# Optimization experiments

Hardware: AMD Instinct MI355X
Metric: run time of the kernel (lower is better)

The kernel has to match this reference:

```python
import jax, jax.numpy as jnp
import numpy as np
from jax import lax

EPS = 1e-10
BN_EPS = 1e-5
T = 0.1
K = 64
B, D, H, Z = 2048, 2048, 512, 500


def _bn(x, g, b):
    # training-mode BatchNorm1d: biased batch stats over axis 0
    mu = x.mean(axis=0)
    var = ((x - mu) ** 2).mean(axis=0)
    return g * (x - mu) / jnp.sqrt(var + BN_EPS) + b


def _leaky(x):
    return jnp.where(x >= 0, x, 0.01 * x)


def setup_inputs() -> dict:
    key = jax.random.key(0)
    ks = jax.random.split(key, 16)
    def lin(k, fan_in, shape):
        return jax.random.normal(k, shape, jnp.float32) / np.sqrt(fan_in)
    return {
        'x': jax.random.uniform(ks[0], (B, D), jnp.float32),
        'u_gumbel': jax.random.uniform(ks[1], (B, D), jnp.float32),
        'eps': jax.random.normal(ks[2], (B, Z), jnp.float32),
        'wc_w1': lin(ks[3], D, (D, H)), 'wc_b1': jnp.zeros((H,)),
        'wc_g': jnp.ones((H,)), 'wc_beta': jnp.zeros((H,)),
        'wc_w2': lin(ks[4], H, (H, D)), 'wc_b2': jnp.zeros((D,)),
        'enc_w1': lin(ks[5], D, (D, 2 * H)), 'enc_b1': jnp.zeros((2 * H,)),
        'enc_g1': jnp.ones((2 * H,)), 'enc_beta1': jnp.zeros((2 * H,)),
        'enc_w2': lin(ks[6], 2 * H, (2 * H, H)), 'enc_b2': jnp.zeros((H,)),
        'enc_g2': jnp.ones((H,)), 'enc_beta2': jnp.zeros((H,)),
        'enc_w3': lin(ks[7], H, (H, H)), 'enc_b3': jnp.zeros((H,)),
        'enc_g3': jnp.ones((H,)), 'enc_beta3': jnp.zeros((H,)),
        'fc21_w': lin(ks[8], H, (H, Z)), 'fc21_b': jnp.zeros((Z,)),
        'fc22_w': lin(ks[9], H, (H, Z)), 'fc22_b': jnp.zeros((Z,)),
        'fc3_w': lin(ks[10], Z, (Z, H)), 'fc3_b': jnp.zeros((H,)),
        'fc3_g': jnp.ones((H,)), 'fc3_beta': jnp.zeros((H,)),
        'fc4_w': lin(ks[11], H, (H, D)), 'fc4_b': jnp.zeros((D,)),
    }


def _sample_subset(w_logits, u):
    # gumbel_keys: w += log(-log(u')) with u' in (EPS, 1)
    u = (1.0 - EPS) * u + EPS
    w = w_logits + jnp.log(-jnp.log(u))

    def step(carry, _):
        w, onehot, acc = carry
        khot_mask = jnp.maximum(1.0 - onehot, EPS)
        w = w + jnp.log(khot_mask)
        onehot = jax.nn.softmax(w / T, axis=-1)
        return (w, onehot, acc + onehot), None

    init = (w, jnp.zeros_like(w), jnp.zeros_like(w))
    (_, _, khot), _ = lax.scan(step, init, None, length=K)
    return khot


def reference(x, u_gumbel, eps,
              wc_w1, wc_b1, wc_g, wc_beta, wc_w2, wc_b2,
              enc_w1, enc_b1, enc_g1, enc_beta1,
              enc_w2, enc_b2, enc_g2, enc_beta2,
              enc_w3, enc_b3, enc_g3, enc_beta3,
              fc21_w, fc21_b, fc22_w, fc22_b,
              fc3_w, fc3_b, fc3_g, fc3_beta, fc4_w, fc4_b):
    # weight_creator: Linear -> BN -> ReLU -> Linear
    h = jax.nn.relu(_bn(x @ wc_w1 + wc_b1, wc_g, wc_beta))
    w_logits = h @ wc_w2 + wc_b2
    khot = _sample_subset(w_logits, u_gumbel)  # [B, D]
    xm = x * khot
    h1 = _leaky(_bn(xm @ enc_w1 + enc_b1, enc_g1, enc_beta1))
    h1 = _leaky(_bn(h1 @ enc_w2 + enc_b2, enc_g2, enc_beta2))
    h1 = _leaky(_bn(h1 @ enc_w3 + enc_b3, enc_g3, enc_beta3))
    mu = h1 @ fc21_w + fc21_b
    logvar = h1 @ fc22_w + fc22_b
    z = mu + eps * jnp.exp(0.5 * logvar)
    hd = _leaky(_bn(z @ fc3_w + fc3_b, fc3_g, fc3_beta))
    mu_x = jax.nn.sigmoid(hd @ fc4_w + fc4_b)
    return (mu_x, mu, logvar)
```

## Files before the change

### kernel.cpp

```cpp
#include <hip/hip_runtime.h>
#include <hip/hip_bf16.h>
#include <math.h>

#define B_DIM 2048
#define D_DIM 2048
#define H_DIM 512
#define Z_DIM 500

#define ACT_NONE 0
#define ACT_RELU 1
#define ACT_SIGMOID 2
#define ACT_LEAKY 3

typedef __attribute__((ext_vector_type(8))) _Float16 f16x8;
typedef __attribute__((ext_vector_type(4))) _Float16 f16x4;
typedef __attribute__((ext_vector_type(4))) float f32x4;
typedef __attribute__((ext_vector_type(2))) float f32x2;

__device__ __forceinline__ float rfl(float x) {
    return __uint_as_float(__builtin_amdgcn_readfirstlane(__float_as_uint(x)));
}

template<int BM, int BN, int TERMS, int BK>
__global__ __launch_bounds__(256, 2) void gemm_f16(
    const _Float16* __restrict__ Ah_, const _Float16* __restrict__ Al_,
    const _Float16* __restrict__ Bh_, const _Float16* __restrict__ Bl_,
    const float* __restrict__ bias, float* __restrict__ C,
    float* __restrict__ part, int M, int N, int K, int act, int Kc)
{
    constexpr int LDK = 40;
    constexpr int NPL = (TERMS == 3) ? 2 : 1;
    constexpr int NCH = BK / 32;
    constexpr int PSA = BM * LDK, PSB = BN * LDK;
    constexpr int CHUNK = NPL * (PSA + PSB);
    constexpr int BUF = NCH * CHUNK;
    constexpr int MT = BM / 32, NT = BN / 32;
    constexpr int CA = BM / 64, CB = BN / 64;
    __shared__ _Float16 smem[2 * BUF];

    const int t = threadIdx.x, lane = t & 63, wv = t >> 6;
    const int wrow = wv >> 1, wcol = wv & 1;
    const int row0 = blockIdx.y * BM, col0 = blockIdx.x * BN;
    const int ks = blockIdx.z * Kc;
    const int nk = Kc / BK;

    f16x8 rA[NCH][CA][NPL], rB[NCH][CB][NPL];

    auto gload = [&](int kt) {
        #pragma unroll
        for (int ch = 0; ch < NCH; ++ch) {
            int kc = kt + ch * 32;
            #pragma unroll
            for (int i = 0; i < CA; ++i) {
                int id = t + i * 256;
                int r = id >> 2, ko = (id & 3) * 8;
                size_t off = (size_t)(row0 + r) * K + kc + ko;
                rA[ch][i][0] = *(const f16x8*)(Ah_ + off);
                if constexpr (TERMS == 3) rA[ch][i][1] = *(const f16x8*)(Al_ + off);
            }
            #pragma unroll
            for (int i = 0; i < CB; ++i) {
                int id = t + i * 256;
                int r = id >> 2, ko = (id & 3) * 8;
                size_t off = (size_t)(col0 + r) * K + kc + ko;
                rB[ch][i][0] = *(const f16x8*)(Bh_ + off);
                if constexpr (TERMS == 3) rB[ch][i][1] = *(const f16x8*)(Bl_ + off);
            }
        }
    };
    auto cstore = [&](int b) {
        #pragma unroll
        for (int ch = 0; ch < NCH; ++ch) {
            _Float16* base = smem + b * BUF + ch * CHUNK;
            #pragma unroll
            for (int i = 0; i < CA; ++i) {
                int id = t + i * 256;
                int r = id >> 2, ko = (id & 3) * 8;
                *(f16x8*)&base[r * LDK + ko] = rA[ch][i][0];
                if constexpr (TERMS == 3) *(f16x8*)&base[PSA + r * LDK + ko] = rA[ch][i][1];
            }
            _Float16* bb = base + NPL * PSA;
            #pragma unroll
            for (int i = 0; i < CB; ++i) {
                int id = t + i * 256;
                int r = id >> 2, ko = (id & 3) * 8;
                *(f16x8*)&bb[r * LDK + ko] = rB[ch][i][0];
                if constexpr (TERMS == 3) *(f16x8*)&bb[PSB + r * LDK + ko] = rB[ch][i][1];
            }
        }
    };

    f32x4 acc[MT][NT];
    #pragma unroll
    for (int i = 0; i < MT; ++i)
        #pragma unroll
        for (int j = 0; j < NT; ++j) {
            f32x4 z = {0.f, 0.f, 0.f, 0.f};
            acc[i][j] = z;
        }

    const int q8 = (lane >> 4) * 8, fr = lane & 15;

    gload(ks);
    cstore(0);
    __syncthreads();

    for (int it = 0; it < nk; ++it) {
        int cur = it & 1;
        if (it + 1 < nk) gload(ks + (it + 1) * BK);

        #pragma unroll
        for (int ch = 0; ch < NCH; ++ch) {
            const _Float16* A0 = smem + cur * BUF + ch * CHUNK;
            const _Float16* A1 = A0 + PSA;
            const _Float16* B0 = A0 + NPL * PSA;
            const _Float16* B1 = B0 + PSB;
            f16x8 ah[MT], al[MT], bh[NT], bl[NT];
            #pragma unroll
            for (int i = 0; i < MT; ++i) {
                int r = wrow * (BM / 2) + i * 16 + fr;
                ah[i] = *(const f16x8*)&A0[r * LDK + q8];
                if constexpr (TERMS == 3) al[i] = *(const f16x8*)&A1[r * LDK + q8];
            }
            #pragma unroll
            for (int j = 0; j < NT; ++j) {
                int n = wcol * (BN / 2) + j * 16 + fr;
                bh[j] = *(const f16x8*)&B0[n * LDK + q8];
                if constexpr (TERMS == 3) bl[j] = *(const f16x8*)&B1[n * LDK + q8];
            }
            #pragma unroll
            for (int i = 0; i < MT; ++i)
                #pragma unroll
                for (int j = 0; j < NT; ++j) {
                    acc[i][j] = __builtin_amdgcn_mfma_f32_16x16x32_f16(ah[i], bh[j], acc[i][j], 0, 0, 0);
                    if constexpr (TERMS == 3) {
                        acc[i][j] = __builtin_amdgcn_mfma_f32_16x16x32_f16(ah[i], bl[j], acc[i][j], 0, 0, 0);
                        acc[i][j] = __builtin_amdgcn_mfma_f32_16x16x32_f16(al[i], bh[j], acc[i][j], 0, 0, 0);
                    }
                }
        }

        if (it + 1 < nk) cstore(cur ^ 1);
        __syncthreads();
    }

    const bool dopart = (gridDim.z > 1);
    float* dst = dopart ? (part + (size_t)blockIdx.z * M * N) : C;
    #pragma unroll
    for (int i = 0; i < MT; ++i) {
        int rbase = row0 + wrow * (BM / 2) + i * 16 + (lane >> 4) * 4;
        #pragma unroll
        for (int j = 0; j < NT; ++j) {
            int c = col0 + wcol * (BN / 2) + j * 16 + (lane & 15);
            if (c < N) {
                float b = dopart ? 0.f : bias[c];
                #pragma unroll
                for (int q = 0; q < 4; ++q) {
                    float v = acc[i][j][q] + b;
                    if (!dopart && act == ACT_SIGMOID)
                        v = 1.f / (1.f + __builtin_amdgcn_exp2f(-v * 1.44269504f));
                    dst[(size_t)(rbase + q) * N + c] = v;
                }
            }
        }
    }
}

__global__ __launch_bounds__(256) void cvt_split_x(
    const float* __restrict__ x, _Float16* __restrict__ xh,
    _Float16* __restrict__ xl, int n4)
{
    int i = blockIdx.x * 256 + threadIdx.x;
    if (i >= n4) return;
    float4 v = ((const float4*)x)[i];
    f16x4 h, l;
    h[0]=(_Float16)v.x; l[0]=(_Float16)(v.x-(float)h[0]);
    h[1]=(_Float16)v.y; l[1]=(_Float16)(v.y-(float)h[1]);
    h[2]=(_Float16)v.z; l[2]=(_Float16)(v.z-(float)h[2]);
    h[3]=(_Float16)v.w; l[3]=(_Float16)(v.w-(float)h[3]);
    ((f16x4*)xh)[i] = h;
    ((f16x4*)xl)[i] = l;
}

__global__ __launch_bounds__(256) void cvt_w_t(
    const float* __restrict__ in, _Float16* __restrict__ outh,
    _Float16* __restrict__ outl, int K, int N, int Kp)
{
    __shared__ float tile[32][33];
    const int t = threadIdx.x;
    const int tk0 = blockIdx.x * 32, tn0 = blockIdx.y * 32;
    const int lx = t & 31, ly = t >> 5;
    #pragma unroll
    for (int r = 0; r < 4; ++r) {
        int k = tk0 + ly + r * 8, n = tn0 + lx;
        tile[ly + r * 8][lx] = (k < K && n < N) ? in[(size_t)k * N + n] : 0.f;
    }
    __syncthreads();
    #pragma unroll
    for (int r = 0; r < 4; ++r) {
        int n = tn0 + ly + r * 8, k = tk0 + lx;
        float v = tile[lx][ly + r * 8];
        _Float16 h = (_Float16)v;
        outh[(size_t)n * Kp + k] = h;
        if (outl) outl[(size_t)n * Kp + k] = (_Float16)(v - (float)h);
    }
}

__global__ __launch_bounds__(256) void reduce_heads(
    const float* __restrict__ part, int S,
    const float* __restrict__ b21, const float* __restrict__ b22,
    float* __restrict__ mu, float* __restrict__ lv)
{
    int i = blockIdx.x * 256 + threadIdx.x;
    const int MN = B_DIM * 1024;
    if (i >= MN) return;
    int row = i >> 10, c = i & 1023;
    float s = 0.f;
    for (int k = 0; k < S; ++k) s += part[(size_t)k * MN + i];
    if (c < Z_DIM) {
        mu[(size_t)row * Z_DIM + c] = s + b21[c];
    } else if (c >= 512 && c < 512 + Z_DIM) {
        lv[(size_t)row * Z_DIM + (c - 512)] = s + b22[c - 512];
    }
}

__global__ __launch_bounds__(256) void reduce_stats(
    const float* __restrict__ part, int S, int Brows, int N, int rowsPerBlock,
    const float* __restrict__ bias, float* __restrict__ Y,
    float* __restrict__ statp)
{
    const int t = threadIdx.x;
    const int col = blockIdx.x * 64 + (t & 63);
    const int g = blockIdx.y;
    const int r0 = g * rowsPerBlock;
    const int r1 = min(r0 + rowsPerBlock, Brows);
    const size_t MN = (size_t)Brows * N;
    const float b = bias[col];
    float s = 0.f, s2 = 0.f;
    for (int r = r0 + (t >> 6); r < r1; r += 4) {
        float v = b;
        for (int k = 0; k < S; ++k) v += part[k * MN + (size_t)r * N + col];
        Y[(size_t)r * N + col] = v;
        s += v;
        s2 += v * v;
    }
    __shared__ float ss[4][64], ss2[4][64];
    ss[t >> 6][t & 63] = s;
    ss2[t >> 6][t & 63] = s2;
    __syncthreads();
    if (t < 64) {
        s  = ss[0][t] + ss[1][t] + ss[2][t] + ss[3][t];
        s2 = ss2[0][t] + ss2[1][t] + ss2[2][t] + ss2[3][t];
        float* p = statp + ((size_t)g * N + col) * 2;
        p[0] = s;
        p[1] = s2;
    }
}

__global__ __launch_bounds__(256) void colstats_final(
    const float* __restrict__ part, int G, int N, int Brows,
    const float* __restrict__ gamma, const float* __restrict__ beta,
    float* __restrict__ scale, float* __restrict__ shift)
{
    int c = blockIdx.x * 256 + threadIdx.x;
    if (c >= N) return;
    float s = 0.f, s2 = 0.f;
    for (int g = 0; g < G; ++g) {
        s  += part[((size_t)g * N + c) * 2];
        s2 += part[((size_t)g * N + c) * 2 + 1];
    }
    float invB = 1.f / (float)Brows;
    float mean = s * invB;
    float var  = s2 * invB - mean * mean;
    float rstd = rsqrtf(var + 1e-5f);
    float sc = gamma[c] * rstd;
    scale[c] = sc;
    shift[c] = beta[c] - mean * sc;
}

__global__ __launch_bounds__(256) void bn_apply_f16(
    const float* __restrict__ Y, const float* __restrict__ scale,
    const float* __restrict__ shift, _Float16* __restrict__ oh,
    _Float16* __restrict__ ol, int total, int N, int act)
{
    int idx = blockIdx.x * 256 + threadIdx.x;
    int i4 = idx * 4;
    if (i4 >= total) return;
    float4 y = *(const float4*)(Y + i4);
    int c = i4 % N;
    float4 sc = *(const float4*)(scale + c);
    float4 sh = *(const float4*)(shift + c);
    float r[4];
    r[0] = y.x * sc.x + sh.x;
    r[1] = y.y * sc.y + sh.y;
    r[2] = y.z * sc.z + sh.z;
    r[3] = y.w * sc.w + sh.w;
    #pragma unroll
    for (int q = 0; q < 4; ++q) {
        if (act == ACT_RELU) r[q] = fmaxf(r[q], 0.f);
        else if (act == ACT_LEAKY) r[q] = (r[q] >= 0.f) ? r[q] : 0.01f * r[q];
    }
    f16x4 h;
    #pragma unroll
    for (int q = 0; q < 4; ++q) h[q] = (_Float16)r[q];
    ((f16x4*)oh)[idx] = h;
    if (ol) {
        f16x4 l;
        #pragma unroll
        for (int q = 0; q < 4; ++q) l[q] = (_Float16)(r[q] - (float)h[q]);
        ((f16x4*)ol)[idx] = l;
    }
}

__global__ __launch_bounds__(256) void gumbel_scan(
    const float* __restrict__ WLg, const float* __restrict__ U,
    const float* __restrict__ X, _Float16* __restrict__ XM)
{
    const int row = blockIdx.x;
    const int t = threadIdx.x, wv = t >> 6, lane = t & 63;
    const float* wrow = WLg + (size_t)row * D_DIM + 8 * t;
    const float* urow = U + (size_t)row * D_DIM + 8 * t;
    const float* xrow = X + (size_t)row * D_DIM + 8 * t;
    _Float16* xmrow = XM + (size_t)row * D_DIM + 8 * t;

    const float L2E = 1.4426950408889634f;
    const float LOG2LN2 = -0.5287663729448977f;

    __shared__ f32x2 sLS[2][4];
    __shared__ float sM0[4];

    f32x2 W2[4], e2[4], acc2[4];

    auto mkW = [&](float wl, float uu) -> float {
        float u = fmaf(uu, 1.0f - 1e-10f, 1e-10f);
        float tl = -__builtin_amdgcn_logf(u);
        return __builtin_amdgcn_exp2f(fmaf(wl, L2E, __builtin_amdgcn_logf(tl) + LOG2LN2));
    };

    {
        float4 ua = *(const float4*)urow, ub = *(const float4*)(urow + 4);
        float4 wa = *(const float4*)wrow, wb = *(const float4*)(wrow + 4);
        W2[0] = f32x2{mkW(wa.x, ua.x), mkW(wa.y, ua.y)};
        W2[1] = f32x2{mkW(wa.z, ua.z), mkW(wa.w, ua.w)};
        W2[2] = f32x2{mkW(wb.x, ub.x), mkW(wb.y, ub.y)};
        W2[3] = f32x2{mkW(wb.z, ub.z), mkW(wb.w, ub.w)};
    }
    #pragma unroll
    for (int j = 0; j < 4; ++j) {
        e2[j] = f32x2{0.f, 0.f};
        acc2[j] = f32x2{0.f, 0.f};
    }

    float rm_s;
    {
        float lm = 0.f;
        #pragma unroll
        for (int j = 0; j < 4; ++j)
            lm = fmaxf(lm, fmaxf(W2[j].x, W2[j].y));
        #pragma unroll
        for (int off = 32; off; off >>= 1)
            lm = fmaxf(lm, __shfl_xor(lm, off));
        if (lane == 0) sM0[wv] = lm;
        __syncthreads();
        float m = fmaxf(fmaxf(sM0[0], sM0[1]), fmaxf(sM0[2], sM0[3]));
        rm_s = rfl(__builtin_amdgcn_rcpf(m));
    }

    float inv_s = 0.f;
    int gi = 0;

    auto iterate = [&](bool refresh) {
        const int p = gi & 1;
        ++gi;
        f32x2 lmv = f32x2{0.f, 0.f}, sv = f32x2{0.f, 0.f};
        #pragma unroll
        for (int j = 0; j < 4; ++j) {
            acc2[j].x = fmaf(e2[j].x, inv_s, acc2[j].x);
            acc2[j].y = fmaf(e2[j].y, inv_s, acc2[j].y);
            f32x2 msk;
            msk.x = fmaxf(fmaf(-e2[j].x, inv_s, 1.0f), 1e-10f);
            msk.y = fmaxf(fmaf(-e2[j].y, inv_s, 1.0f), 1e-10f);
            f32x2 Wn = W2[j] * msk;
            W2[j] = Wn;
            f32x2 r;
            r.x = Wn.x * rm_s;
            r.y = Wn.y * rm_s;
            f32x2 q2 = r * r;
            f32x2 q4 = q2 * q2;
            f32x2 q8 = q4 * q4;
            f32x2 ee = q8 * q2;
            e2[j] = ee;
            sv += ee;
            if (refresh) {
                lmv.x = fmaxf(lmv.x, Wn.x);
                lmv.y = fmaxf(lmv.y, Wn.y);
            }
        }
        float s = sv.x + sv.y;
        if (refresh) {
            float lm = fmaxf(lmv.x, lmv.y);
            #pragma unroll
            for (int off = 32; off; off >>= 1) {
                s += __shfl_xor(s, off);
                lm = fmaxf(lm, __shfl_xor(lm, off));
            }
            if (lane == 0) sLS[p][wv] = f32x2{lm, s};
            __syncthreads();
            f32x2 r0 = sLS[p][0], r1 = sLS[p][1], r2 = sLS[p][2], r3 = sLS[p][3];
            float m = fmaxf(fmaxf(r0.x, r1.x), fmaxf(r2.x, r3.x));
            float st = (r0.y + r1.y) + (r2.y + r3.y);
            rm_s = rfl(__builtin_amdgcn_rcpf(m));
            inv_s = rfl(__builtin_amdgcn_rcpf(st));
        } else {
            #pragma unroll
            for (int off = 32; off; off >>= 1)
                s += __shfl_xor(s, off);
            if (lane == 0) sLS[p][wv].y = s;
            __syncthreads();
            float st = (sLS[p][0].y + sLS[p][1].y) + (sLS[p][2].y + sLS[p][3].y);
            inv_s = rfl(__builtin_amdgcn_rcpf(st));
        }
    };

    for (int ot = 0; ot < 16; ++ot) {
        iterate(false);
        iterate(false);
        iterate(false);
        iterate(true);
    }

    {
        float4 xa = *(const float4*)xrow, xb = *(const float4*)(xrow + 4);
        f32x2 a0, a1, a2, a3;
        a0.x = fmaf(e2[0].x, inv_s, acc2[0].x); a0.y = fmaf(e2[0].y, inv_s, acc2[0].y);
        a1.x = fmaf(e2[1].x, inv_s, acc2[1].x); a1.y = fmaf(e2[1].y, inv_s, acc2[1].y);
        a2.x = fmaf(e2[2].x, inv_s, acc2[2].x); a2.y = fmaf(e2[2].y, inv_s, acc2[2].y);
        a3.x = fmaf(e2[3].x, inv_s, acc2[3].x); a3.y = fmaf(e2[3].y, inv_s, acc2[3].y);
        f16x8 o;
        o[0] = (_Float16)(xa.x * a0.x);
        o[1] = (_Float16)(xa.y * a0.y);
        o[2] = (_Float16)(xa.z * a1.x);
        o[3] = (_Float16)(xa.w * a1.y);
        o[4] = (_Float16)(xb.x * a2.x);
        o[5] = (_Float16)(xb.y * a2.y);
        o[6] = (_Float16)(xb.z * a3.x);
        o[7] = (_Float16)(xb.w * a3.y);
        *(f16x8*)xmrow = o;
    }
}

__global__ __launch_bounds__(256) void z_kernel16(
    const float* __restrict__ mu, const float* __restrict__ lv,
    const float* __restrict__ eps, _Float16* __restrict__ zb, int n4)
{
    int i = blockIdx.x * 256 + threadIdx.x;
    if (i >= n4) return;
    int f = i * 4;
    int row = f / Z_DIM, col = f - row * Z_DIM;
    float4 m = *(const float4*)(mu + f);
    float4 l = *(const float4*)(lv + f);
    float4 e = *(const float4*)(eps + f);
    const float HL2E = 0.7213475204444817f;
    f16x4 r;
    r[0] = (_Float16)(m.x + e.x * __builtin_amdgcn_exp2f(l.x * HL2E));
    r[1] = (_Float16)(m.y + e.y * __builtin_amdgcn_exp2f(l.y * HL2E));
    r[2] = (_Float16)(m.z + e.z * __builtin_amdgcn_exp2f(l.z * HL2E));
    r[3] = (_Float16)(m.w + e.w * __builtin_amdgcn_exp2f(l.w * HL2E));
    *(f16x4*)(zb + (size_t)row * 512 + col) = r;
}

extern "C" void kernel_launch(void* const* d_in, const int* in_sizes, int n_in,
                              void* d_out, int out_size, void* d_ws, size_t ws_size,
                              hipStream_t stream) {
    const float* x        = (const float*)d_in[0];
    const float* u_gumbel = (const float*)d_in[1];
    const float* eps      = (const float*)d_in[2];
    const float* wc_w1    = (const float*)d_in[3];
    const float* wc_b1    = (const float*)d_in[4];
    const float* wc_g     = (const float*)d_in[5];
    const float* wc_beta  = (const float*)d_in[6];
    const float* wc_w2    = (const float*)d_in[7];
    const float* wc_b2    = (const float*)d_in[8];
    const float* enc_w1   = (const float*)d_in[9];
    const float* enc_b1   = (const float*)d_in[10];
    const float* enc_g1   = (const float*)d_in[11];
    const float* enc_beta1= (const float*)d_in[12];
    const float* enc_w2   = (const float*)d_in[13];
    const float* enc_b2   = (const float*)d_in[14];
    const float* enc_g2   = (const float*)d_in[15];
    const float* enc_beta2= (const float*)d_in[16];
    const float* enc_w3   = (const float*)d_in[17];
    const float* enc_b3   = (const float*)d_in[18];
    const float* enc_g3   = (const float*)d_in[19];
    const float* enc_beta3= (const float*)d_in[20];
    const float* fc21_w   = (const float*)d_in[21];
    const float* fc21_b   = (const float*)d_in[22];
    const float* fc22_w   = (const float*)d_in[23];
    const float* fc22_b   = (const float*)d_in[24];
    const float* fc3_w    = (const float*)d_in[25];
    const float* fc3_b    = (const float*)d_in[26];
    const float* fc3_g    = (const float*)d_in[27];
    const float* fc3_beta = (const float*)d_in[28];
    const float* fc4_w    = (const float*)d_in[29];
    const float* fc4_b    = (const float*)d_in[30];

    float* out   = (float*)d_out;
    float* mu_x  = out;
    float* mu    = out + (size_t)B_DIM * D_DIM;
    float* lv    = mu + (size_t)B_DIM * Z_DIM;

    const size_t F1M = 1u << 20;
    float* wsf = (float*)d_ws;
    float*     P_WL  = wsf;
    _Float16*  xh    = (_Float16*)(wsf + 4 * F1M);
    _Float16*  xl    = (_Float16*)(wsf + 6 * F1M);
    _Float16*  xm16  = (_Float16*)(wsf + 4 * F1M);
    float*     Yb    = wsf + 6 * F1M;
    _Float16*  a2    = (_Float16*)(wsf + 8 * F1M);
    _Float16*  a3    = (_Float16*)(wsf + 9 * F1M);
    _Float16*  a4    = (_Float16*)(wsf + 9 * F1M + F1M / 2);
    _Float16*  zb16  = (_Float16*)(wsf + 10 * F1M);
    _Float16*  a5    = (_Float16*)(wsf + 10 * F1M + F1M / 2);
    float*     Hbuf  = wsf + 11 * F1M;
    _Float16*  Hh    = (_Float16*)(wsf + 12 * F1M);
    _Float16*  Hl    = (_Float16*)(wsf + 12 * F1M + F1M / 2);
    _Float16*  w1th  = (_Float16*)(wsf + 13 * F1M);
    _Float16*  w1tl  = (_Float16*)(wsf + 13 * F1M + F1M / 2);
    _Float16*  w2th  = (_Float16*)(wsf + 14 * F1M);
    _Float16*  w2tl  = (_Float16*)(wsf + 14 * F1M + F1M / 2);
    _Float16*  e1t   = (_Float16*)(wsf + 15 * F1M);
    _Float16*  e2t   = (_Float16*)(wsf + 16 * F1M);
    _Float16*  e3t   = (_Float16*)(wsf + 16 * F1M + F1M / 4);
    _Float16*  f21t  = (_Float16*)(wsf + 16 * F1M + 3 * (F1M / 8));
    _Float16*  f22t  = (_Float16*)(wsf + 16 * F1M + 4 * (F1M / 8));
    _Float16*  f3t   = (_Float16*)(wsf + 16 * F1M + 5 * (F1M / 8));
    _Float16*  f4t   = (_Float16*)(wsf + 16 * F1M + 6 * (F1M / 8));
    float*     bnp   = wsf + 17 * F1M + F1M / 4;
    float*     scale = bnp + 131072;
    float*     shift = scale + 2048;

    const int G = 64;

    auto gemm3 = [&](const _Float16* Ah, const _Float16* Al,
                     const _Float16* Bh, const _Float16* Bl,
                     const float* b, float* C, float* part,
                     int N, int K, int SK) {
        dim3 grid((N + 63) / 64, B_DIM / 128, SK);
        gemm_f16<128, 64, 3, 32><<<grid, 256, 0, stream>>>(Ah, Al, Bh, Bl, b, C, part,
                                                           B_DIM, N, K, ACT_NONE, K / SK);
    };
    auto gemm1 = [&](const _Float16* Ah, const _Float16* Bh,
                     const float* b, float* C, float* part,
                     int N, int K, int act, int SK) {
        dim3 grid((N + 63) / 64, B_DIM / 128, SK);
        gemm_f16<128, 64, 1, 64><<<grid, 256, 0, stream>>>(Ah, nullptr, Bh, nullptr, b, C,
                                                           part, B_DIM, N, K, act, K / SK);
    };
    auto bnFromParts = [&](const float* part, int S, const float* b,
                           const float* g_, const float* beta_,
                           float* Y, _Float16* oh, _Float16* ol, int N, int act) {
        dim3 gp(N / 64, G);
        reduce_stats<<<gp, 256, 0, stream>>>(part, S, B_DIM, N, B_DIM / G, b, Y, bnp);
        colstats_final<<<(N + 255) / 256, 256, 0, stream>>>(bnp, G, N, B_DIM, g_, beta_, scale, shift);
        int total = B_DIM * N;
        bn_apply_f16<<<(total / 4 + 255) / 256, 256, 0, stream>>>(Y, scale, shift, oh, ol, total, N, act);
    };
    auto cvtw = [&](const float* in, _Float16* oh, _Float16* ol, int K, int N, int Kp, int Np) {
        dim3 grid(Kp / 32, Np / 32);
        cvt_w_t<<<grid, 256, 0, stream>>>(in, oh, ol, K, N, Kp);
    };

    cvt_split_x<<<4096, 256, 0, stream>>>(x, xh, xl, B_DIM * D_DIM / 4);
    cvtw(wc_w1, w1th, w1tl, 2048, 512, 2048, 512);
    cvtw(wc_w2, w2th, w2tl, 512, 2048, 512, 2048);
    cvtw(enc_w1, e1t, nullptr, 2048, 1024, 2048, 1024);
    cvtw(enc_w2, e2t, nullptr, 1024, 512, 1024, 512);
    cvtw(enc_w3, e3t, nullptr, 512, 512, 512, 512);
    cvtw(fc21_w, f21t, nullptr, 512, 500, 512, 512);
    cvtw(fc22_w, f22t, nullptr, 512, 500, 512, 512);
    cvtw(fc3_w, f3t, nullptr, 500, 512, 512, 512);
    cvtw(fc4_w, f4t, nullptr, 512, 2048, 512, 2048);

    gemm3(xh, xl, w1th, w1tl, nullptr, nullptr, P_WL, 512, 2048, 4);
    bnFromParts(P_WL, 4, wc_b1, wc_g, wc_beta, Hbuf, Hh, Hl, 512, ACT_RELU);
    gemm3(Hh, Hl, w2th, w2tl, wc_b2, P_WL, nullptr, 2048, 512, 1);

    gumbel_scan<<<B_DIM, 256, 0, stream>>>(P_WL, u_gumbel, x, xm16);

    gemm1(xm16, e1t, nullptr, nullptr, P_WL, 1024, 2048, ACT_NONE, 2);
    bnFromParts(P_WL, 2, enc_b1, enc_g1, enc_beta1, Yb, a2, nullptr, 1024, ACT_LEAKY);
    gemm1(a2, e2t, nullptr, nullptr, P_WL, 512, 1024, ACT_NONE, 4);
    bnFromParts(P_WL, 4, enc_b2, enc_g2, enc_beta2, Yb, a3, nullptr, 512, ACT_LEAKY);
    gemm1(a3, e3t, nullptr, nullptr, P_WL, 512, 512, ACT_NONE, 4);
    bnFromParts(P_WL, 4, enc_b3, enc_g3, enc_beta3, Yb, a4, nullptr, 512, ACT_LEAKY);

    gemm1(a4, f21t, nullptr, nullptr, P_WL, 1024, 512, ACT_NONE, 4);
    {
        int MN = B_DIM * 1024;
        reduce_heads<<<(MN + 255) / 256, 256, 0, stream>>>(P_WL, 4, fc21_b, fc22_b, mu, lv);
    }

    hipMemsetAsync(zb16, 0, (size_t)B_DIM * 512 * sizeof(_Float16), stream);
    int n4 = B_DIM * Z_DIM / 4;
    z_kernel16<<<(n4 + 255) / 256, 256, 0, stream>>>(mu, lv, eps, zb16, n4);

    gemm1(zb16, f3t, nullptr, nullptr, P_WL, 512, 512, ACT_NONE, 4);
    bnFromParts(P_WL, 4, fc3_b, fc3_g, fc3_beta, Yb, a5, nullptr, 512, ACT_LEAKY);
    gemm1(a5, f4t, fc4_b, mu_x, nullptr, 2048, 512, ACT_SIGMOID, 1);
}
```

Measured before the change: 422.3 us.

## Process two rows per gumbel-scan block and fuse head reduction with z sampling

```diff
diff --git a/kernel.cpp b/kernel.cpp
--- a/kernel.cpp
+++ b/kernel.cpp
@@ -206,21 +206,31 @@
     }
 }
 
-__global__ __launch_bounds__(256) void reduce_heads(
+__global__ __launch_bounds__(256) void reduce_heads_z(
     const float* __restrict__ part, int S,
     const float* __restrict__ b21, const float* __restrict__ b22,
-    float* __restrict__ mu, float* __restrict__ lv)
+    const float* __restrict__ eps, float* __restrict__ mu,
+    float* __restrict__ lv, _Float16* __restrict__ zb)
 {
     int i = blockIdx.x * 256 + threadIdx.x;
-    const int MN = B_DIM * 1024;
-    if (i >= MN) return;
-    int row = i >> 10, c = i & 1023;
-    float s = 0.f;
-    for (int k = 0; k < S; ++k) s += part[(size_t)k * MN + i];
+    if (i >= B_DIM * 512) return;
+    int row = i >> 9, c = i & 511;
     if (c < Z_DIM) {
-        mu[(size_t)row * Z_DIM + c] = s + b21[c];
-    } else if (c >= 512 && c < 512 + Z_DIM) {
-        lv[(size_t)row * Z_DIM + (c - 512)] = s + b22[c - 512];
+        const size_t MN = (size_t)B_DIM * 1024;
+        size_t ia = (size_t)row * 1024 + c;
+        float sm = b21[c], sl = b22[c];
+        for (int k = 0; k < S; ++k) {
+            sm += part[k * MN + ia];
+            sl += part[k * MN + ia + 512];
+        }
+        size_t o = (size_t)row * Z_DIM + c;
+        mu[o] = sm;
+        lv[o] = sl;
+        const float HL2E = 0.7213475204444817f;
+        zb[(size_t)row * 512 + c] =
+            (_Float16)(sm + eps[o] * __builtin_amdgcn_exp2f(sl * HL2E));
+    } else {
+        zb[(size_t)row * 512 + c] = (_Float16)0.f;
     }
 }
 
@@ -316,20 +326,21 @@
     const float* __restrict__ WLg, const float* __restrict__ U,
     const float* __restrict__ X, _Float16* __restrict__ XM)
 {
-    const int row = blockIdx.x;
     const int t = threadIdx.x, wv = t >> 6, lane = t & 63;
-    const float* wrow = WLg + (size_t)row * D_DIM + 8 * t;
-    const float* urow = U + (size_t)row * D_DIM + 8 * t;
-    const float* xrow = X + (size_t)row * D_DIM + 8 * t;
-    _Float16* xmrow = XM + (size_t)row * D_DIM + 8 * t;
+    const size_t base = (size_t)(blockIdx.x * 2) * D_DIM + 8 * t;
+    const float* wA = WLg + base;  const float* wB = wA + D_DIM;
+    const float* uA = U + base;    const float* uB = uA + D_DIM;
+    const float* xA = X + base;    const float* xB = xA + D_DIM;
+    _Float16* oA = XM + base;      _Float16* oB = oA + D_DIM;
 
     const float L2E = 1.4426950408889634f;
     const float LOG2LN2 = -0.5287663729448977f;
 
-    __shared__ f32x2 sLS[2][4];
-    __shared__ float sM0[4];
-
-    f32x2 W2[4], e2[4], acc2[4];
+    __shared__ f32x4 sLS[2][4];
+    __shared__ f32x2 sM0[4];
+
+    f32x2 WA[4], eA[4], aA[4];
+    f32x2 WB[4], eB[4], aB[4];
 
     auto mkW = [&](float wl, float uu) -> float {
         float u = fmaf(uu, 1.0f - 1e-10f, 1e-10f);
@@ -338,87 +349,110 @@
     };
 
     {
-        float4 ua = *(const float4*)urow, ub = *(const float4*)(urow + 4);
-        float4 wa = *(const float4*)wrow, wb = *(const float4*)(wrow + 4);
-        W2[0] = f32x2{mkW(wa.x, ua.x), mkW(wa.y, ua.y)};
-        W2[1] = f32x2{mkW(wa.z, ua.z), mkW(wa.w, ua.w)};
-        W2[2] = f32x2{mkW(wb.x, ub.x), mkW(wb.y, ub.y)};
-        W2[3] = f32x2{mkW(wb.z, ub.z), mkW(wb.w, ub.w)};
+        float4 u4a = *(const float4*)uA, u4b = *(const float4*)(uA + 4);
+        float4 w4a = *(const float4*)wA, w4b = *(const float4*)(wA + 4);
+        WA[0] = f32x2{mkW(w4a.x, u4a.x), mkW(w4a.y, u4a.y)};
+        WA[1] = f32x2{mkW(w4a.z, u4a.z), mkW(w4a.w, u4a.w)};
+        WA[2] = f32x2{mkW(w4b.x, u4b.x), mkW(w4b.y, u4b.y)};
+        WA[3] = f32x2{mkW(w4b.z, u4b.z), mkW(w4b.w, u4b.w)};
+        u4a = *(const float4*)uB; u4b = *(const float4*)(uB + 4);
+        w4a = *(const float4*)wB; w4b = *(const float4*)(wB + 4);
+        WB[0] = f32x2{mkW(w4a.x, u4a.x), mkW(w4a.y, u4a.y)};
+        WB[1] = f32x2{mkW(w4a.z, u4a.z), mkW(w4a.w, u4a.w)};
+        WB[2] = f32x2{mkW(w4b.x, u4b.x), mkW(w4b.y, u4b.y)};
+        WB[3] = f32x2{mkW(w4b.z, u4b.z), mkW(w4b.w, u4b.w)};
     }
     #pragma unroll
     for (int j = 0; j < 4; ++j) {
-        e2[j] = f32x2{0.f, 0.f};
-        acc2[j] = f32x2{0.f, 0.f};
-    }
-
-    float rm_s;
+        eA[j] = f32x2{0.f, 0.f}; aA[j] = f32x2{0.f, 0.f};
+        eB[j] = f32x2{0.f, 0.f}; aB[j] = f32x2{0.f, 0.f};
+    }
+
+    float rmA, rmB;
     {
-        float lm = 0.f;
-        #pragma unroll
-        for (int j = 0; j < 4; ++j)
-            lm = fmaxf(lm, fmaxf(W2[j].x, W2[j].y));
-        #pragma unroll
-        for (int off = 32; off; off >>= 1)
-            lm = fmaxf(lm, __shfl_xor(lm, off));
-        if (lane == 0) sM0[wv] = lm;
+        float la = 0.f, lb = 0.f;
+        #pragma unroll
+        for (int j = 0; j < 4; ++j) {
+            la = fmaxf(la, fmaxf(WA[j].x, WA[j].y));
+            lb = fmaxf(lb, fmaxf(WB[j].x, WB[j].y));
+        }
+        #pragma unroll
+        for (int off = 32; off; off >>= 1) {
+            la = fmaxf(la, __shfl_xor(la, off));
+            lb = fmaxf(lb, __shfl_xor(lb, off));
+        }
+        if (lane == 0) sM0[wv] = f32x2{la, lb};
         __syncthreads();
-        float m = fmaxf(fmaxf(sM0[0], sM0[1]), fmaxf(sM0[2], sM0[3]));
-        rm_s = rfl(__builtin_amdgcn_rcpf(m));
-    }
-
-    float inv_s = 0.f;
+        f32x2 m0 = sM0[0], m1 = sM0[1], m2 = sM0[2], m3 = sM0[3];
+        rmA = rfl(__builtin_amdgcn_rcpf(fmaxf(fmaxf(m0.x, m1.x), fmaxf(m2.x, m3.x))));
+        rmB = rfl(__builtin_amdgcn_rcpf(fmaxf(fmaxf(m0.y, m1.y), fmaxf(m2.y, m3.y))));
+    }
+
+    float invA = 0.f, invB = 0.f;
     int gi = 0;
 
     auto iterate = [&](bool refresh) {
         const int p = gi & 1;
         ++gi;
-        f32x2 lmv = f32x2{0.f, 0.f}, sv = f32x2{0.f, 0.f};
+        f32x2 lvA = f32x2{0.f, 0.f}, svA = f32x2{0.f, 0.f};
+        f32x2 lvB = f32x2{0.f, 0.f}, svB = f32x2{0.f, 0.f};
         #pragma unroll
         for (int j = 0; j < 4; ++j) {
-            acc2[j].x = fmaf(e2[j].x, inv_s, acc2[j].x);
-            acc2[j].y = fmaf(e2[j].y, inv_s, acc2[j].y);
-            f32x2 msk;
-            msk.x = fmaxf(fmaf(-e2[j].x, inv_s, 1.0f), 1e-10f);
-            msk.y = fmaxf(fmaf(-e2[j].y, inv_s, 1.0f), 1e-10f);
-            f32x2 Wn = W2[j] * msk;
-            W2[j] = Wn;
+            aA[j].x = fmaf(eA[j].x, invA, aA[j].x);
+            aA[j].y = fmaf(eA[j].y, invA, aA[j].y);
+            f32x2 mk;
+            mk.x = fmaxf(fmaf(-eA[j].x, invA, 1.0f), 1e-10f);
+            mk.y = fmaxf(fmaf(-eA[j].y, invA, 1.0f), 1e-10f);
+            f32x2 Wn = WA[j] * mk;
+            WA[j] = Wn;
             f32x2 r;
-            r.x = Wn.x * rm_s;
-            r.y = Wn.y * rm_s;
-            f32x2 q2 = r * r;
-            f32x2 q4 = q2 * q2;
-            f32x2 q8 = q4 * q4;
+            r.x = Wn.x * rmA; r.y = Wn.y * rmA;
+            f32x2 q2 = r * r, q4 = q2 * q2, q8 = q4 * q4;
             f32x2 ee = q8 * q2;
-            e2[j] = ee;
-            sv += ee;
-            if (refresh) {
-                lmv.x = fmaxf(lmv.x, Wn.x);
-                lmv.y = fmaxf(lmv.y, Wn.y);
-            }
-        }
-        float s = sv.x + sv.y;
+            eA[j] = ee;
+            svA += ee;
+            if (refresh) { lvA.x = fmaxf(lvA.x, Wn.x); lvA.y = fmaxf(lvA.y, Wn.y); }
+            aB[j].x = fmaf(eB[j].x, invB, aB[j].x);
+            aB[j].y = fmaf(eB[j].y, invB, aB[j].y);
+            mk.x = fmaxf(fmaf(-eB[j].x, invB, 1.0f), 1e-10f);
+            mk.y = fmaxf(fmaf(-eB[j].y, invB, 1.0f), 1e-10f);
+            Wn = WB[j] * mk;
+            WB[j] = Wn;
+            r.x = Wn.x * rmB; r.y = Wn.y * rmB;
+            q2 = r * r; q4 = q2 * q2; q8 = q4 * q4;
+            ee = q8 * q2;
+            eB[j] = ee;
+            svB += ee;
+            if (refresh) { lvB.x = fmaxf(lvB.x, Wn.x); lvB.y = fmaxf(lvB.y, Wn.y); }
+        }
+        float sa = svA.x + svA.y, sb = svB.x + svB.y;
         if (refresh) {
-            float lm = fmaxf(lmv.x, lmv.y);
+            float la = fmaxf(lvA.x, lvA.y), lb = fmaxf(lvB.x, lvB.y);
             #pragma unroll
             for (int off = 32; off; off >>= 1) {
-                s += __shfl_xor(s, off);
-                lm = fmaxf(lm, __shfl_xor(lm, off));
-            }
-            if (lane == 0) sLS[p][wv] = f32x2{lm, s};
+                sa += __shfl_xor(sa, off);
+                sb += __shfl_xor(sb, off);
+                la = fmaxf(la, __shfl_xor(la, off));
+                lb = fmaxf(lb, __shfl_xor(lb, off));
+            }
+            if (lane == 0) sLS[p][wv] = f32x4{la, sa, lb, sb};
             __syncthreads();
-            f32x2 r0 = sLS[p][0], r1 = sLS[p][1], r2 = sLS[p][2], r3 = sLS[p][3];
-            float m = fmaxf(fmaxf(r0.x, r1.x), fmaxf(r2.x, r3.x));
-            float st = (r0.y + r1.y) + (r2.y + r3.y);
-            rm_s = rfl(__builtin_amdgcn_rcpf(m));
-            inv_s = rfl(__builtin_amdgcn_rcpf(st));
+            f32x4 r0 = sLS[p][0], r1 = sLS[p][1], r2 = sLS[p][2], r3 = sLS[p][3];
+            rmA = rfl(__builtin_amdgcn_rcpf(fmaxf(fmaxf(r0[0], r1[0]), fmaxf(r2[0], r3[0]))));
+            invA = rfl(__builtin_amdgcn_rcpf((r0[1] + r1[1]) + (r2[1] + r3[1])));
+            rmB = rfl(__builtin_amdgcn_rcpf(fmaxf(fmaxf(r0[2], r1[2]), fmaxf(r2[2], r3[2]))));
+            invB = rfl(__builtin_amdgcn_rcpf((r0[3] + r1[3]) + (r2[3] + r3[3])));
         } else {
             #pragma unroll
-            for (int off = 32; off; off >>= 1)
-                s += __shfl_xor(s, off);
-            if (lane == 0) sLS[p][wv].y = s;
+            for (int off = 32; off; off >>= 1) {
+                sa += __shfl_xor(sa, off);
+                sb += __shfl_xor(sb, off);
+            }
+            if (lane == 0) { sLS[p][wv][1] = sa; sLS[p][wv][3] = sb; }
             __syncthreads();
-            float st = (sLS[p][0].y + sLS[p][1].y) + (sLS[p][2].y + sLS[p][3].y);
-            inv_s = rfl(__builtin_amdgcn_rcpf(st));
+            f32x4 r0 = sLS[p][0], r1 = sLS[p][1], r2 = sLS[p][2], r3 = sLS[p][3];
+            invA = rfl(__builtin_amdgcn_rcpf((r0[1] + r1[1]) + (r2[1] + r3[1])));
+            invB = rfl(__builtin_amdgcn_rcpf((r0[3] + r1[3]) + (r2[3] + r3[3])));
         }
     };
 
@@ -430,43 +464,28 @@
     }
 
     {
-        float4 xa = *(const float4*)xrow, xb = *(const float4*)(xrow + 4);
-        f32x2 a0, a1, a2, a3;
-        a0.x = fmaf(e2[0].x, inv_s, acc2[0].x); a0.y = fmaf(e2[0].y, inv_s, acc2[0].y);
-        a1.x = fmaf(e2[1].x, inv_s, acc2[1].x); a1.y = fmaf(e2[1].y, inv_s, acc2[1].y);
-        a2.x = fmaf(e2[2].x, inv_s, acc2[2].x); a2.y = fmaf(e2[2].y, inv_s, acc2[2].y);
-        a3.x = fmaf(e2[3].x, inv_s, acc2[3].x); a3.y = fmaf(e2[3].y, inv_s, acc2[3].y);
+        float4 xa = *(const float4*)xA, xb = *(const float4*)(xA + 4);
         f16x8 o;
-        o[0] = (_Float16)(xa.x * a0.x);
-        o[1] = (_Float16)(xa.y * a0.y);
-        o[2] = (_Float16)(xa.z * a1.x);
-        o[3] = (_Float16)(xa.w * a1.y);
-        o[4] = (_Float16)(xb.x * a2.x);
-        o[5] = (_Float16)(xb.y * a2.y);
-        o[6] = (_Float16)(xb.z * a3.x);
-        o[7] = (_Float16)(xb.w * a3.y);
-        *(f16x8*)xmrow = o;
-    }
-}
-
-__global__ __launch_bounds__(256) void z_kernel16(
-    const float* __restrict__ mu, const float* __restrict__ lv,
-    const float* __restrict__ eps, _Float16* __restrict__ zb, int n4)
-{
-    int i = blockIdx.x * 256 + threadIdx.x;
-    if (i >= n4) return;
-    int f = i * 4;
-    int row = f / Z_DIM, col = f - row * Z_DIM;
-    float4 m = *(const float4*)(mu + f);
-    float4 l = *(const float4*)(lv + f);
-    float4 e = *(const float4*)(eps + f);
-    const float HL2E = 0.7213475204444817f;
-    f16x4 r;
-    r[0] = (_Float16)(m.x + e.x * __builtin_amdgcn_exp2f(l.x * HL2E));
-    r[1] = (_Float16)(m.y + e.y * __builtin_amdgcn_exp2f(l.y * HL2E));
-    r[2] = (_Float16)(m.z + e.z * __builtin_amdgcn_exp2f(l.z * HL2E));
-    r[3] = (_Float16)(m.w + e.w * __builtin_amdgcn_exp2f(l.w * HL2E));
-    *(f16x4*)(zb + (size_t)row * 512 + col) = r;
+        o[0] = (_Float16)(xa.x * fmaf(eA[0].x, invA, aA[0].x));
+        o[1] = (_Float16)(xa.y * fmaf(eA[0].y, invA, aA[0].y));
+        o[2] = (_Float16)(xa.z * fmaf(eA[1].x, invA, aA[1].x));
+        o[3] = (_Float16)(xa.w * fmaf(eA[1].y, invA, aA[1].y));
+        o[4] = (_Float16)(xb.x * fmaf(eA[2].x, invA, aA[2].x));
+        o[5] = (_Float16)(xb.y * fmaf(eA[2].y, invA, aA[2].y));
+        o[6] = (_Float16)(xb.z * fmaf(eA[3].x, invA, aA[3].x));
+        o[7] = (_Float16)(xb.w * fmaf(eA[3].y, invA, aA[3].y));
+        *(f16x8*)oA = o;
+        xa = *(const float4*)xB; xb = *(const float4*)(xB + 4);
+        o[0] = (_Float16)(xa.x * fmaf(eB[0].x, invB, aB[0].x));
+        o[1] = (_Float16)(xa.y * fmaf(eB[0].y, invB, aB[0].y));
+        o[2] = (_Float16)(xa.z * fmaf(eB[1].x, invB, aB[1].x));
+        o[3] = (_Float16)(xa.w * fmaf(eB[1].y, invB, aB[1].y));
+        o[4] = (_Float16)(xb.x * fmaf(eB[2].x, invB, aB[2].x));
+        o[5] = (_Float16)(xb.y * fmaf(eB[2].y, invB, aB[2].y));
+        o[6] = (_Float16)(xb.z * fmaf(eB[3].x, invB, aB[3].x));
+        o[7] = (_Float16)(xb.w * fmaf(eB[3].y, invB, aB[3].y));
+        *(f16x8*)oB = o;
+    }
 }
 
 extern "C" void kernel_launch(void* const* d_in, const int* in_sizes, int n_in,
@@ -585,7 +604,7 @@
     bnFromParts(P_WL, 4, wc_b1, wc_g, wc_beta, Hbuf, Hh, Hl, 512, ACT_RELU);
     gemm3(Hh, Hl, w2th, w2tl, wc_b2, P_WL, nullptr, 2048, 512, 1);
 
-    gumbel_scan<<<B_DIM, 256, 0, stream>>>(P_WL, u_gumbel, x, xm16);
+    gumbel_scan<<<B_DIM / 2, 256, 0, stream>>>(P_WL, u_gumbel, x, xm16);
 
     gemm1(xm16, e1t, nullptr, nullptr, P_WL, 1024, 2048, ACT_NONE, 2);
     bnFromParts(P_WL, 2, enc_b1, enc_g1, enc_beta1, Yb, a2, nullptr, 1024, ACT_LEAKY);
@@ -595,14 +614,8 @@
     bnFromParts(P_WL, 4, enc_b3, enc_g3, enc_beta3, Yb, a4, nullptr, 512, ACT_LEAKY);
 
     gemm1(a4, f21t, nullptr, nullptr, P_WL, 1024, 512, ACT_NONE, 4);
-    {
-        int MN = B_DIM * 1024;
-        reduce_heads<<<(MN + 255) / 256, 256, 0, stream>>>(P_WL, 4, fc21_b, fc22_b, mu, lv);
-    }
-
-    hipMemsetAsync(zb16, 0, (size_t)B_DIM * 512 * sizeof(_Float16), stream);
-    int n4 = B_DIM * Z_DIM / 4;
-    z_kernel16<<<(n4 + 255) / 256, 256, 0, stream>>>(mu, lv, eps, zb16, n4);
+    reduce_heads_z<<<(B_DIM * 512 + 255) / 256, 256, 0, stream>>>(
+        P_WL, 4, fc21_b, fc22_b, eps, mu, lv, zb16);
 
     gemm1(zb16, f3t, nullptr, nullptr, P_WL, 512, 512, ACT_NONE, 4);
     bnFromParts(P_WL, 4, fc3_b, fc3_g, fc3_beta, Yb, a5, nullptr, 512, ACT_LEAKY);
```

Measured after the change: 432.0 us. 2.3% more time.
